# Optimization experiments

Measured on AMD Instinct MI355X. Metric: run time of the kernel, lower is better.

The kernel has to match this reference:

```python
import jax, jax.numpy as jnp
import numpy as np

N = 100000
IN_C = 128
OUT_C = 32
HEADS = 4
E = 1600000
NEG_SLOPE = 0.2


def setup_inputs() -> dict:
    key = jax.random.key(0)
    ks = jax.random.split(key, 8)
    x = jax.random.normal(ks[0], (N, IN_C), dtype=jnp.float32)
    edge_index = jax.random.randint(ks[1], (2, E), 0, N, dtype=jnp.int64)
    # GATConv params (PyG conventions): lin weight [H*C, in], att vectors [H, C], bias [H*C]
    sc = 1.0 / np.sqrt(IN_C)
    W = jax.random.uniform(ks[2], (HEADS * OUT_C, IN_C), dtype=jnp.float32, minval=-sc, maxval=sc)
    att_src = jax.random.normal(ks[3], (HEADS, OUT_C), dtype=jnp.float32) * 0.1
    att_dst = jax.random.normal(ks[4], (HEADS, OUT_C), dtype=jnp.float32) * 0.1
    bias_conv = jnp.zeros((HEADS * OUT_C,), dtype=jnp.float32)
    # final nn.Linear(H*C, C)
    sl = 1.0 / np.sqrt(HEADS * OUT_C)
    W_lin = jax.random.uniform(ks[5], (OUT_C, HEADS * OUT_C), dtype=jnp.float32, minval=-sl, maxval=sl)
    b_lin = jax.random.uniform(ks[6], (OUT_C,), dtype=jnp.float32, minval=-sl, maxval=sl)
    return {"x": x, "edge_index": edge_index, "W": W, "att_src": att_src,
            "att_dst": att_dst, "bias_conv": bias_conv, "W_lin": W_lin, "b_lin": b_lin}


def reference(x, edge_index, W, att_src, att_dst, bias_conv, W_lin, b_lin):
    n = x.shape[0]
    # add self loops (PyG default)
    loops = jnp.arange(n, dtype=edge_index.dtype)
    src = jnp.concatenate([edge_index[0], loops])
    dst = jnp.concatenate([edge_index[1], loops])
    # linear projection, per-head split: [N, H, C]
    h = (x @ W.T).reshape(n, HEADS, OUT_C)
    # per-node attention logits
    a_src = jnp.einsum('nhc,hc->nh', h, att_src)  # [N, H]
    a_dst = jnp.einsum('nhc,hc->nh', h, att_dst)  # [N, H]
    e = a_src[src] + a_dst[dst]                   # [E', H]
    e = jax.nn.leaky_relu(e, NEG_SLOPE)
    # segment softmax over incoming edges per destination node
    m = jax.ops.segment_max(e, dst, num_segments=n)       # [N, H]
    e = jnp.exp(e - m[dst])
    s = jax.ops.segment_sum(e, dst, num_segments=n)       # [N, H]
    alpha = e / s[dst]                                    # [E', H]
    # scatter-aggregate alpha-weighted source features
    msg = alpha[:, :, None] * h[src]                      # [E', H, C]
    out = jax.ops.segment_sum(msg, dst, num_segments=n)   # [N, H, C]
    out = out.reshape(n, HEADS * OUT_C) + bias_conv
    # final linear + ELU
    return jax.nn.elu(out @ W_lin.T + b_lin)
```

## Files before the change

kernel.cpp:

```cpp
#include <hip/hip_runtime.h>
#include <hip/hip_fp16.h>
#include <cstdint>
#include <cstddef>

#define NHEADS 4
#define OUT_C 32
#define HC 128
#define IN_CH 128
#define NEG_SLOPE 0.2f
#define LDSPAD 136
#define KEDGE 4096

typedef _Float16 half8 __attribute__((ext_vector_type(8)));
typedef float floatx4 __attribute__((ext_vector_type(4)));

static inline size_t align256(size_t v) { return (v + 255) & ~(size_t)255; }

__device__ __forceinline__ float lrelu(float v) { return v > 0.f ? v : NEG_SLOPE * v; }

__device__ __forceinline__ float wred_sum(float v) {
    v += __shfl_xor(v, 1);
    v += __shfl_xor(v, 2);
    v += __shfl_xor(v, 4);
    v += __shfl_xor(v, 8);
    v += __shfl_xor(v, 16);
    v += __shfl_xor(v, 32);
    return v;
}

__device__ __forceinline__ unsigned int pack_h2(float a, float b) {
    __half2 h = __floats2half2_rn(a, b);
    return *reinterpret_cast<unsigned int*>(&h);
}
__device__ __forceinline__ float2 unpack_h2(unsigned int u) {
    __half2 h = *reinterpret_cast<__half2*>(&u);
    return __half22float2(h);
}

__device__ __forceinline__ int detect_f64(const int* __restrict__ ei, int E, int* sf) {
    int t = threadIdx.x;
    if (t == 0) *sf = 0;
    __syncthreads();
    int lim = E < 1024 ? E : 1024;
    int acc = 0;
    for (int i = t; i < lim; i += 256) acc |= ei[2 * i + 1];
    acc |= __shfl_xor(acc, 1);
    acc |= __shfl_xor(acc, 2);
    acc |= __shfl_xor(acc, 4);
    acc |= __shfl_xor(acc, 8);
    acc |= __shfl_xor(acc, 16);
    acc |= __shfl_xor(acc, 32);
    if ((t & 63) == 0 && acc) atomicOr(sf, 1);
    __syncthreads();
    return *sf == 0;
}

__global__ __launch_bounds__(256) void gemm_hist(const float* __restrict__ x,
                                                 const float* __restrict__ W,
                                                 const float* __restrict__ att_src,
                                                 const float* __restrict__ att_dst,
                                                 __half* __restrict__ h,
                                                 float* __restrict__ a_src,
                                                 float* __restrict__ a_dst, int n,
                                                 const int* __restrict__ ei,
                                                 int* __restrict__ bcount,
                                                 int E, int sh, int GB) {
    __shared__ __align__(16) _Float16 Ws[128 * LDSPAD];
    __shared__ __align__(16) _Float16 Xs[128 * LDSPAD];
    __shared__ int hc[256];
    __shared__ int sf;
    int tid = threadIdx.x;

    if (blockIdx.x >= GB) {
        hc[tid] = 0;
        int f64 = detect_f64(ei, E, &sf);
        int nbh = gridDim.x - GB;
        int stride = nbh * 256;
        for (int i = (blockIdx.x - GB) * 256 + tid; i < E; i += stride) {
            int d;
            if (f64) d = (int)((const long long*)ei)[(size_t)E + i];
            else     d = ei[(size_t)E + i];
            atomicAdd(&hc[d >> sh], 1);
        }
        __syncthreads();
        if (hc[tid]) atomicAdd(&bcount[tid], hc[tid]);
        return;
    }
    int rowbase = blockIdx.x << 7;

    const float4* wf = (const float4*)W;
#pragma unroll
    for (int i = 0; i < 16; ++i) {
        int u = (i << 8) + tid;
        int r = u >> 5, g = u & 31;
        float4 v = wf[u];
        uint2 uu;
        uu.x = pack_h2(v.x, v.y);
        uu.y = pack_h2(v.z, v.w);
        *(uint2*)&Ws[r * LDSPAD + (g << 2)] = uu;
    }
    const float4* x4 = (const float4*)x;
#pragma unroll
    for (int i = 0; i < 16; ++i) {
        int u = (i << 8) + tid;
        int r = u >> 5, c4 = u & 31;
        int row = rowbase + r;
        if (row >= n) row = n - 1;
        float4 v = x4[((size_t)row << 5) + c4];
        uint2 uu;
        uu.x = pack_h2(v.x, v.y);
        uu.y = pack_h2(v.z, v.w);
        *(uint2*)&Xs[r * LDSPAD + (c4 << 2)] = uu;
    }
    __syncthreads();

    int lane = tid & 63, w = tid >> 6;
    int quad = lane >> 4, Lm = lane & 15;
    floatx4 acc[2][8];
#pragma unroll
    for (int rt = 0; rt < 2; ++rt)
#pragma unroll
        for (int c = 0; c < 8; ++c) acc[rt][c] = (floatx4){0.f, 0.f, 0.f, 0.f};

#pragma unroll
    for (int kc = 0; kc < 128; kc += 32) {
        int ko = kc + (quad << 3);
        half8 a0 = *(const half8*)&Xs[((w << 5) + Lm) * LDSPAD + ko];
        half8 a1 = *(const half8*)&Xs[((w << 5) + 16 + Lm) * LDSPAD + ko];
#pragma unroll
        for (int c = 0; c < 8; ++c) {
            half8 b = *(const half8*)&Ws[((c << 4) + Lm) * LDSPAD + ko];
            acc[0][c] = __builtin_amdgcn_mfma_f32_16x16x32_f16(a0, b, acc[0][c], 0, 0, 0);
            acc[1][c] = __builtin_amdgcn_mfma_f32_16x16x32_f16(a1, b, acc[1][c], 0, 0, 0);
        }
    }
    __syncthreads();
#pragma unroll
    for (int rt = 0; rt < 2; ++rt)
#pragma unroll
        for (int c = 0; c < 8; ++c)
#pragma unroll
            for (int i = 0; i < 4; ++i) {
                int rl = (w << 5) + (rt << 4) + (quad << 2) + i;
                int cl = (c << 4) + Lm;
                Xs[rl * LDSPAD + cl] = (_Float16)acc[rt][c][i];
            }
    __syncthreads();
#pragma unroll
    for (int i = 0; i < 8; ++i) {
        int u = (i << 8) + tid;
        int r = u >> 4, g = u & 15;
        int row = rowbase + r;
        if (row < n) {
            uint4 v = *(uint4*)&Xs[r * LDSPAD + (g << 3)];
            *(uint4*)(h + ((size_t)row << 7) + (g << 3)) = v;
        }
    }
    int r = tid >> 1, seg = tid & 1;
    int row = rowbase + r;
    const _Float16* hp = &Xs[r * LDSPAD + (seg << 6)];
    float sa = 0.f, da = 0.f, sb = 0.f, db = 0.f;
#pragma unroll
    for (int g8 = 0; g8 < 8; ++g8) {
        half8 v = *(const half8*)&hp[g8 << 3];
        int co = (seg << 6) + (g8 << 3);
        float4 A1 = *(const float4*)&att_src[co];
        float4 A2 = *(const float4*)&att_src[co + 4];
        float4 D1 = *(const float4*)&att_dst[co];
        float4 D2 = *(const float4*)&att_dst[co + 4];
        float f0 = (float)v[0], f1 = (float)v[1], f2 = (float)v[2], f3 = (float)v[3];
        float f4 = (float)v[4], f5 = (float)v[5], f6 = (float)v[6], f7 = (float)v[7];
        float ts = f0 * A1.x + f1 * A1.y + f2 * A1.z + f3 * A1.w
                 + f4 * A2.x + f5 * A2.y + f6 * A2.z + f7 * A2.w;
        float td = f0 * D1.x + f1 * D1.y + f2 * D1.z + f3 * D1.w
                 + f4 * D2.x + f5 * D2.y + f6 * D2.z + f7 * D2.w;
        if (g8 < 4) { sa += ts; da += td; } else { sb += ts; db += td; }
    }
    if (row < n) {
        int base = (row << 2) + (seg << 1);
        a_src[base] = sa;
        a_src[base + 1] = sb;
        a_dst[base] = da;
        a_dst[base + 1] = db;
    }
}

__global__ __launch_bounds__(256) void bscatter(const int* __restrict__ ei,
                                                const int* __restrict__ bcount,
                                                int* __restrict__ gcursor,
                                                int2* __restrict__ bkt,
                                                int E, int n, int sh) {
    __shared__ int cnt[256], base[256], lcur[256], ts[256];
    __shared__ int sf;
    int t = threadIdx.x;
    cnt[t] = 0;
    lcur[t] = 0;
    int f64 = detect_f64(ei, E, &sf);
    int total = E + n;
    int i0 = blockIdx.x * KEDGE;
    int ed[16], es[16];
#pragma unroll
    for (int j = 0; j < 16; ++j) {
        int i = i0 + (j << 8) + t;
        int s = 0, d = -1;
        if (i < total) {
            if (i < E) {
                if (f64) {
                    s = (int)((const long long*)ei)[i];
                    d = (int)((const long long*)ei)[(size_t)E + i];
                } else {
                    s = ei[i];
                    d = ei[(size_t)E + i];
                }
            } else {
                s = d = i - E;
            }
            atomicAdd(&cnt[d >> sh], 1);
        }
        ed[j] = d;
        es[j] = s;
    }
    int lo = t << sh, hi = (t + 1) << sh;
    if (hi > n) hi = n;
    int nodes = hi > lo ? hi - lo : 0;
    int v = bcount[t] + nodes;
    ts[t] = v;
    __syncthreads();
    int run = v;
    for (int d = 1; d < 256; d <<= 1) {
        int o = (t >= d) ? ts[t - d] : 0;
        __syncthreads();
        run += o;
        ts[t] = run;
        __syncthreads();
    }
    int excl = run - v;
    base[t] = excl + (cnt[t] ? atomicAdd(&gcursor[t], cnt[t]) : 0);
    __syncthreads();
#pragma unroll
    for (int j = 0; j < 16; ++j) {
        int d = ed[j];
        if (d >= 0) {
            int b = d >> sh;
            int pos = base[b] + atomicAdd(&lcur[b], 1);
            bkt[pos] = make_int2(d, es[j]);
        }
    }
}

__global__ __launch_bounds__(256) void bsort(const int2* __restrict__ bkt,
                                             const int* __restrict__ bcount,
                                             int* __restrict__ off,
                                             int* __restrict__ sorted,
                                             int n, int E, int sh) {
    __shared__ int cnt[512], offl[512], ts[256];
    int t = threadIdx.x, bid = blockIdx.x;
    int lo = t << sh, hi = (t + 1) << sh;
    if (hi > n) hi = n;
    int nodes = hi > lo ? hi - lo : 0;
    int v = bcount[t] + nodes;
    ts[t] = v;
    __syncthreads();
    int run = v;
    for (int d = 1; d < 256; d <<= 1) {
        int o = (t >= d) ? ts[t - d] : 0;
        __syncthreads();
        run += o;
        ts[t] = run;
        __syncthreads();
    }
    int e0 = (bid > 0) ? ts[bid - 1] : 0;
    int e1 = ts[bid];
    if (bid == gridDim.x - 1 && t == 0) off[n] = E + n;
    int node0 = bid << sh;
    int node1 = (bid + 1) << sh;
    if (node1 > n) node1 = n;
    int nn = node1 - node0;
    __syncthreads();
    cnt[t] = 0;
    cnt[t + 256] = 0;
    __syncthreads();
    for (int i = e0 + t; i < e1; i += 256) {
        int2 e = bkt[i];
        atomicAdd(&cnt[e.x - node0], 1);
    }
    __syncthreads();
    int a = cnt[t << 1], b = cnt[(t << 1) + 1];
    int s = a + b;
    ts[t] = s;
    __syncthreads();
    run = s;
    for (int d = 1; d < 256; d <<= 1) {
        int o = (t >= d) ? ts[t - d] : 0;
        __syncthreads();
        run += o;
        ts[t] = run;
        __syncthreads();
    }
    int excl = run - s;
    offl[t << 1] = excl;
    offl[(t << 1) + 1] = excl + a;
    cnt[t << 1] = 0;
    cnt[(t << 1) + 1] = 0;
    __syncthreads();
    for (int i = t; i < nn; i += 256) off[node0 + i] = e0 + offl[i];
    for (int i = e0 + t; i < e1; i += 256) {
        int2 e = bkt[i];
        int li = e.x - node0;
        int pos = e0 + offl[li] + atomicAdd(&cnt[li], 1);
        sorted[pos] = e.y;
    }
}

__device__ __forceinline__ void accum_half(const int* ssrc, const float* sal,
                                           const __half* __restrict__ h,
                                           int deg, int half, int L, int head,
                                           float4& acc) {
    float4 a0 = {0, 0, 0, 0}, a1 = {0, 0, 0, 0}, a2 = {0, 0, 0, 0}, a3 = {0, 0, 0, 0};
    int j = half;
    for (; j + 14 < deg; j += 16) {
        int s0 = ssrc[j], s1 = ssrc[j + 2], s2 = ssrc[j + 4], s3 = ssrc[j + 6];
        int s4 = ssrc[j + 8], s5 = ssrc[j + 10], s6 = ssrc[j + 12], s7 = ssrc[j + 14];
        float w0 = sal[(j << 2) + head];
        float w1 = sal[((j + 2) << 2) + head];
        float w2 = sal[((j + 4) << 2) + head];
        float w3 = sal[((j + 6) << 2) + head];
        float w4 = sal[((j + 8) << 2) + head];
        float w5 = sal[((j + 10) << 2) + head];
        float w6 = sal[((j + 12) << 2) + head];
        float w7 = sal[((j + 14) << 2) + head];
        uint2 u0 = *(const uint2*)(h + ((size_t)s0 << 7) + (L << 2));
        uint2 u1 = *(const uint2*)(h + ((size_t)s1 << 7) + (L << 2));
        uint2 u2 = *(const uint2*)(h + ((size_t)s2 << 7) + (L << 2));
        uint2 u3 = *(const uint2*)(h + ((size_t)s3 << 7) + (L << 2));
        uint2 u4 = *(const uint2*)(h + ((size_t)s4 << 7) + (L << 2));
        uint2 u5 = *(const uint2*)(h + ((size_t)s5 << 7) + (L << 2));
        uint2 u6 = *(const uint2*)(h + ((size_t)s6 << 7) + (L << 2));
        uint2 u7 = *(const uint2*)(h + ((size_t)s7 << 7) + (L << 2));
        float2 fa, fb;
        fa = unpack_h2(u0.x); fb = unpack_h2(u0.y);
        a0.x = fmaf(w0, fa.x, a0.x); a0.y = fmaf(w0, fa.y, a0.y);
        a0.z = fmaf(w0, fb.x, a0.z); a0.w = fmaf(w0, fb.y, a0.w);
        fa = unpack_h2(u1.x); fb = unpack_h2(u1.y);
        a1.x = fmaf(w1, fa.x, a1.x); a1.y = fmaf(w1, fa.y, a1.y);
        a1.z = fmaf(w1, fb.x, a1.z); a1.w = fmaf(w1, fb.y, a1.w);
        fa = unpack_h2(u2.x); fb = unpack_h2(u2.y);
        a2.x = fmaf(w2, fa.x, a2.x); a2.y = fmaf(w2, fa.y, a2.y);
        a2.z = fmaf(w2, fb.x, a2.z); a2.w = fmaf(w2, fb.y, a2.w);
        fa = unpack_h2(u3.x); fb = unpack_h2(u3.y);
        a3.x = fmaf(w3, fa.x, a3.x); a3.y = fmaf(w3, fa.y, a3.y);
        a3.z = fmaf(w3, fb.x, a3.z); a3.w = fmaf(w3, fb.y, a3.w);
        fa = unpack_h2(u4.x); fb = unpack_h2(u4.y);
        a0.x = fmaf(w4, fa.x, a0.x); a0.y = fmaf(w4, fa.y, a0.y);
        a0.z = fmaf(w4, fb.x, a0.z); a0.w = fmaf(w4, fb.y, a0.w);
        fa = unpack_h2(u5.x); fb = unpack_h2(u5.y);
        a1.x = fmaf(w5, fa.x, a1.x); a1.y = fmaf(w5, fa.y, a1.y);
        a1.z = fmaf(w5, fb.x, a1.z); a1.w = fmaf(w5, fb.y, a1.w);
        fa = unpack_h2(u6.x); fb = unpack_h2(u6.y);
        a2.x = fmaf(w6, fa.x, a2.x); a2.y = fmaf(w6, fa.y, a2.y);
        a2.z = fmaf(w6, fb.x, a2.z); a2.w = fmaf(w6, fb.y, a2.w);
        fa = unpack_h2(u7.x); fb = unpack_h2(u7.y);
        a3.x = fmaf(w7, fa.x, a3.x); a3.y = fmaf(w7, fa.y, a3.y);
        a3.z = fmaf(w7, fb.x, a3.z); a3.w = fmaf(w7, fb.y, a3.w);
    }
    for (; j + 6 < deg; j += 8) {
        int s0 = ssrc[j], s1 = ssrc[j + 2], s2 = ssrc[j + 4], s3 = ssrc[j + 6];
        float w0 = sal[(j << 2) + head];
        float w1 = sal[((j + 2) << 2) + head];
        float w2 = sal[((j + 4) << 2) + head];
        float w3 = sal[((j + 6) << 2) + head];
        uint2 u0 = *(const uint2*)(h + ((size_t)s0 << 7) + (L << 2));
        uint2 u1 = *(const uint2*)(h + ((size_t)s1 << 7) + (L << 2));
        uint2 u2 = *(const uint2*)(h + ((size_t)s2 << 7) + (L << 2));
        uint2 u3 = *(const uint2*)(h + ((size_t)s3 << 7) + (L << 2));
        float2 fa, fb;
        fa = unpack_h2(u0.x); fb = unpack_h2(u0.y);
        a0.x = fmaf(w0, fa.x, a0.x); a0.y = fmaf(w0, fa.y, a0.y);
        a0.z = fmaf(w0, fb.x, a0.z); a0.w = fmaf(w0, fb.y, a0.w);
        fa = unpack_h2(u1.x); fb = unpack_h2(u1.y);
        a1.x = fmaf(w1, fa.x, a1.x); a1.y = fmaf(w1, fa.y, a1.y);
        a1.z = fmaf(w1, fb.x, a1.z); a1.w = fmaf(w1, fb.y, a1.w);
        fa = unpack_h2(u2.x); fb = unpack_h2(u2.y);
        a2.x = fmaf(w2, fa.x, a2.x); a2.y = fmaf(w2, fa.y, a2.y);
        a2.z = fmaf(w2, fb.x, a2.z); a2.w = fmaf(w2, fb.y, a2.w);
        fa = unpack_h2(u3.x); fb = unpack_h2(u3.y);
        a3.x = fmaf(w3, fa.x, a3.x); a3.y = fmaf(w3, fa.y, a3.y);
        a3.z = fmaf(w3, fb.x, a3.z); a3.w = fmaf(w3, fb.y, a3.w);
    }
    for (; j < deg; j += 2) {
        int s0 = ssrc[j];
        float w0 = sal[(j << 2) + head];
        uint2 u0 = *(const uint2*)(h + ((size_t)s0 << 7) + (L << 2));
        float2 fa = unpack_h2(u0.x), fb = unpack_h2(u0.y);
        a0.x = fmaf(w0, fa.x, a0.x); a0.y = fmaf(w0, fa.y, a0.y);
        a0.z = fmaf(w0, fb.x, a0.z); a0.w = fmaf(w0, fb.y, a0.w);
    }
    acc.x += (a0.x + a1.x) + (a2.x + a3.x);
    acc.y += (a0.y + a1.y) + (a2.y + a3.y);
    acc.z += (a0.z + a1.z) + (a2.z + a3.z);
    acc.w += (a0.w + a1.w) + (a2.w + a3.w);
}

__global__ __launch_bounds__(256) void aggregate(const __half* __restrict__ h,
                                                 const int* __restrict__ sorted,
                                                 const int* __restrict__ off,
                                                 const float* __restrict__ a_src,
                                                 const float* __restrict__ a_dst,
                                                 const float* __restrict__ bias,
                                                 __half* __restrict__ agg, int n) {
    __shared__ __align__(16) int sh_src[4][64];
    __shared__ __align__(16) float sh_al[4][256];
    int wslot = threadIdx.x >> 6;
    int lane = threadIdx.x & 63;
    int wid = blockIdx.x * 4 + wslot;
    int nw = gridDim.x * 4;
    int L = lane & 31, half = lane >> 5, head = L >> 3;
    float4 b4 = ((const float4*)bias)[L];
    const float4* as4 = (const float4*)a_src;
    const float4* ad4 = (const float4*)a_dst;
    int* ssrc = sh_src[wslot];
    float* sal = sh_al[wslot];

    for (int node = wid; node < n; node += nw) {
        int start = off[node], end = off[node + 1];
        int deg = end - start;
        float4 ad = ad4[node];
        float4 acc = {0.f, 0.f, 0.f, 0.f};
        float4 psum = {0.f, 0.f, 0.f, 0.f};

        if (deg <= 64) {
            bool v = lane < deg;
            int idx = start + (v ? lane : 0);
            int s = sorted[idx];
            float4 as = as4[s];
            float4 p;
            p.x = v ? __expf(lrelu(as.x + ad.x)) : 0.f;
            p.y = v ? __expf(lrelu(as.y + ad.y)) : 0.f;
            p.z = v ? __expf(lrelu(as.z + ad.z)) : 0.f;
            p.w = v ? __expf(lrelu(as.w + ad.w)) : 0.f;
            psum = p;
            ssrc[lane] = s;
            *(float4*)&sal[lane << 2] = p;
            asm volatile("s_waitcnt lgkmcnt(0)" ::: "memory");
            accum_half(ssrc, sal, h, deg, half, L, head, acc);
            asm volatile("" ::: "memory");
        } else {
            for (int bb = 0; bb < deg; bb += 64) {
                int i = bb + lane;
                bool v = i < deg;
                int idx = start + (v ? i : 0);
                int s = sorted[idx];
                float4 as = as4[s];
                float4 p;
                p.x = v ? __expf(lrelu(as.x + ad.x)) : 0.f;
                p.y = v ? __expf(lrelu(as.y + ad.y)) : 0.f;
                p.z = v ? __expf(lrelu(as.z + ad.z)) : 0.f;
                p.w = v ? __expf(lrelu(as.w + ad.w)) : 0.f;
                psum.x += p.x; psum.y += p.y; psum.z += p.z; psum.w += p.w;
                ssrc[lane] = s;
                *(float4*)&sal[lane << 2] = p;
                asm volatile("s_waitcnt lgkmcnt(0)" ::: "memory");
                int cl = deg - bb;
                if (cl > 64) cl = 64;
                accum_half(ssrc, sal, h, cl, half, L, head, acc);
                asm volatile("" ::: "memory");
            }
        }
        float s0 = wred_sum(psum.x), s1 = wred_sum(psum.y);
        float s2 = wred_sum(psum.z), s3 = wred_sum(psum.w);
        float sh = (head == 0) ? s0 : (head == 1) ? s1 : (head == 2) ? s2 : s3;
        float inv = 1.f / sh;
        acc.x += __shfl_xor(acc.x, 32);
        acc.y += __shfl_xor(acc.y, 32);
        acc.z += __shfl_xor(acc.z, 32);
        acc.w += __shfl_xor(acc.w, 32);
        if (lane < 32) {
            float4 res = {fmaf(acc.x, inv, b4.x), fmaf(acc.y, inv, b4.y),
                          fmaf(acc.z, inv, b4.z), fmaf(acc.w, inv, b4.w)};
            uint2 u;
            u.x = pack_h2(res.x, res.y);
            u.y = pack_h2(res.z, res.w);
            *(uint2*)(agg + ((size_t)node << 7) + (L << 2)) = u;
        }
    }
}

__global__ __launch_bounds__(256) void proj(const __half* __restrict__ agg,
                                            const float* __restrict__ W_lin,
                                            const float* __restrict__ b_lin,
                                            float* __restrict__ out, int n) {
    __shared__ float xs[64][132];
    __shared__ float wt[128][36];
    int tid = threadIdx.x;
    const float4* w4 = (const float4*)W_lin;
#pragma unroll
    for (int i = 0; i < 4; ++i) {
        int f4 = (i << 8) + tid;
        int o = f4 >> 5, kk = (f4 & 31) << 2;
        float4 w = w4[f4];
        wt[kk][o] = w.x;
        wt[kk + 1][o] = w.y;
        wt[kk + 2][o] = w.z;
        wt[kk + 3][o] = w.w;
    }
    int rowbase = blockIdx.x << 6;
    const uint4* a4 = (const uint4*)agg;
#pragma unroll
    for (int i = 0; i < 4; ++i) {
        int f8 = (i << 8) + tid;
        int r = f8 >> 4, cc = (f8 & 15) << 3;
        int row = rowbase + r;
        if (row >= n) row = n - 1;
        uint4 u = a4[((size_t)row << 4) + (cc >> 3)];
        float2 f0 = unpack_h2(u.x), f1 = unpack_h2(u.y);
        float2 f2 = unpack_h2(u.z), f3 = unpack_h2(u.w);
        float* xp = &xs[r][cc];
        xp[0] = f0.x; xp[1] = f0.y; xp[2] = f1.x; xp[3] = f1.y;
        xp[4] = f2.x; xp[5] = f2.y; xp[6] = f3.x; xp[7] = f3.y;
    }
    __syncthreads();
    int r = tid >> 2, cg = tid & 3, c0 = cg << 3;
    float acc[8];
#pragma unroll
    for (int j = 0; j < 8; ++j) acc[j] = 0.f;
    for (int k = 0; k < 128; k += 4) {
        float4 xv = *(const float4*)&xs[r][k];
        float xk[4] = {xv.x, xv.y, xv.z, xv.w};
#pragma unroll
        for (int kk = 0; kk < 4; ++kk) {
            float4 wa = *(const float4*)&wt[k + kk][c0];
            float4 wb = *(const float4*)&wt[k + kk][c0 + 4];
            acc[0] = fmaf(xk[kk], wa.x, acc[0]);
            acc[1] = fmaf(xk[kk], wa.y, acc[1]);
            acc[2] = fmaf(xk[kk], wa.z, acc[2]);
            acc[3] = fmaf(xk[kk], wa.w, acc[3]);
            acc[4] = fmaf(xk[kk], wb.x, acc[4]);
            acc[5] = fmaf(xk[kk], wb.y, acc[5]);
            acc[6] = fmaf(xk[kk], wb.z, acc[6]);
            acc[7] = fmaf(xk[kk], wb.w, acc[7]);
        }
    }
    int row = rowbase + r;
    if (row < n) {
        float res[8];
#pragma unroll
        for (int j = 0; j < 8; ++j) {
            float v = acc[j] + b_lin[c0 + j];
            res[j] = v > 0.f ? v : (__expf(v) - 1.f);
        }
        float4* op = (float4*)(out + (size_t)row * 32 + c0);
        op[0] = make_float4(res[0], res[1], res[2], res[3]);
        op[1] = make_float4(res[4], res[5], res[6], res[7]);
    }
}

extern "C" void kernel_launch(void* const* d_in, const int* in_sizes, int n_in,
                              void* d_out, int out_size, void* d_ws, size_t ws_size,
                              hipStream_t stream) {
    const float* x = (const float*)d_in[0];
    const int* ei = (const int*)d_in[1];
    const float* W = (const float*)d_in[2];
    const float* att_src = (const float*)d_in[3];
    const float* att_dst = (const float*)d_in[4];
    const float* bias_conv = (const float*)d_in[5];
    const float* W_lin = (const float*)d_in[6];
    const float* b_lin = (const float*)d_in[7];
    int n = in_sizes[0] / IN_CH;
    int E = in_sizes[1] / 2;

    int sh = 0;
    while (((n + (1 << sh) - 1) >> sh) > 256) sh++;
    int NB = (n + (1 << sh) - 1) >> sh;

    char* ws = (char*)d_ws;
    size_t o = 0;
    auto alloc = [&](size_t bytes) { char* p = ws + o; o = align256(o + bytes); return p; };
    __half* h      = (__half*)alloc((size_t)n * HC * 2);
    __half* agg    = (__half*)alloc((size_t)n * HC * 2);
    float* a_src   = (float*)alloc((size_t)n * NHEADS * 4);
    float* a_dst   = (float*)alloc((size_t)n * NHEADS * 4);
    int* off       = (int*)alloc(((size_t)n + 1) * 4);
    int* bcount    = (int*)alloc(256 * 4);
    int* gcursor   = (int*)alloc(256 * 4);
    int* sorted    = (int*)alloc((size_t)(E + n + 64) * 4);
    int2* bkt      = (int2*)alloc((size_t)(E + n + 64) * 8);

    hipMemsetAsync(bcount, 0, 2048, stream);

    int GB = (n + 127) / 128;
    int NBH = 1024;
    gemm_hist<<<GB + NBH, 256, 0, stream>>>(x, W, att_src, att_dst, h, a_src, a_dst, n,
                                            ei, bcount, E, sh, GB);
    bscatter<<<(E + n + KEDGE - 1) / KEDGE, 256, 0, stream>>>(ei, bcount, gcursor, bkt, E, n, sh);
    bsort<<<NB, 256, 0, stream>>>(bkt, bcount, off, sorted, n, E, sh);
    aggregate<<<2048, 256, 0, stream>>>(h, sorted, off, a_src, a_dst, bias_conv, agg, n);
    proj<<<(n + 63) / 64, 256, 0, stream>>>(agg, W_lin, b_lin, (float*)d_out, n);
}
```

Baseline: 294.6 us.

## Precompute edge attention weights in bsort and store packed edge records

Moves the per-edge attention logit computation (a_src gather, leaky-relu, exp) from the aggregate kernel into the bucket sort kernel. The sort writes 16-byte records holding the source index and fp16-packed exp weights, with a_dst staged in shared memory. Aggregate then reads one contiguous record instead of a dependent random gather of a_src, which removes a latency chain from the hot loop. In exchange the sorted buffer grows from 4 to 16 bytes per edge, so more memory traffic, and the unnormalized weights are stored in fp16 without the max subtraction, so large logits could overflow.

Measured after the change: 307.0 us. +4.2%, slower.

```diff
diff --git a/kernel.cpp b/kernel.cpp
--- a/kernel.cpp
+++ b/kernel.cpp
@@ -250,10 +250,13 @@
 
 __global__ __launch_bounds__(256) void bsort(const int2* __restrict__ bkt,
                                              const int* __restrict__ bcount,
+                                             const float* __restrict__ a_src,
+                                             const float* __restrict__ a_dst,
                                              int* __restrict__ off,
-                                             int* __restrict__ sorted,
+                                             int4* __restrict__ recs,
                                              int n, int E, int sh) {
     __shared__ int cnt[512], offl[512], ts[256];
+    __shared__ __align__(16) float sad[512 * 4];
     int t = threadIdx.x, bid = blockIdx.x;
     int lo = t << sh, hi = (t + 1) << sh;
     if (hi > n) hi = n;
@@ -279,6 +282,9 @@
     __syncthreads();
     cnt[t] = 0;
     cnt[t + 256] = 0;
+    const float4* ad4 = (const float4*)a_dst;
+    for (int i = t; i < nn; i += 256)
+        *(float4*)&sad[i << 2] = ad4[node0 + i];
     __syncthreads();
     for (int i = e0 + t; i < e1; i += 256) {
         int2 e = bkt[i];
@@ -304,11 +310,19 @@
     cnt[(t << 1) + 1] = 0;
     __syncthreads();
     for (int i = t; i < nn; i += 256) off[node0 + i] = e0 + offl[i];
+    const float4* as4 = (const float4*)a_src;
     for (int i = e0 + t; i < e1; i += 256) {
         int2 e = bkt[i];
         int li = e.x - node0;
+        float4 as = as4[e.y];
+        float4 ad = *(const float4*)&sad[li << 2];
+        int4 rec;
+        rec.x = e.y;
+        rec.y = (int)pack_h2(__expf(lrelu(as.x + ad.x)), __expf(lrelu(as.y + ad.y)));
+        rec.z = (int)pack_h2(__expf(lrelu(as.z + ad.z)), __expf(lrelu(as.w + ad.w)));
+        rec.w = 0;
         int pos = e0 + offl[li] + atomicAdd(&cnt[li], 1);
-        sorted[pos] = e.y;
+        recs[pos] = rec;
     }
 }
 
@@ -402,10 +416,8 @@
 }
 
 __global__ __launch_bounds__(256) void aggregate(const __half* __restrict__ h,
-                                                 const int* __restrict__ sorted,
+                                                 const int4* __restrict__ recs,
                                                  const int* __restrict__ off,
-                                                 const float* __restrict__ a_src,
-                                                 const float* __restrict__ a_dst,
                                                  const float* __restrict__ bias,
                                                  __half* __restrict__ agg, int n) {
     __shared__ __align__(16) int sh_src[4][64];
@@ -416,30 +428,25 @@
     int nw = gridDim.x * 4;
     int L = lane & 31, half = lane >> 5, head = L >> 3;
     float4 b4 = ((const float4*)bias)[L];
-    const float4* as4 = (const float4*)a_src;
-    const float4* ad4 = (const float4*)a_dst;
     int* ssrc = sh_src[wslot];
     float* sal = sh_al[wslot];
 
     for (int node = wid; node < n; node += nw) {
         int start = off[node], end = off[node + 1];
         int deg = end - start;
-        float4 ad = ad4[node];
         float4 acc = {0.f, 0.f, 0.f, 0.f};
         float4 psum = {0.f, 0.f, 0.f, 0.f};
 
         if (deg <= 64) {
             bool v = lane < deg;
             int idx = start + (v ? lane : 0);
-            int s = sorted[idx];
-            float4 as = as4[s];
-            float4 p;
-            p.x = v ? __expf(lrelu(as.x + ad.x)) : 0.f;
-            p.y = v ? __expf(lrelu(as.y + ad.y)) : 0.f;
-            p.z = v ? __expf(lrelu(as.z + ad.z)) : 0.f;
-            p.w = v ? __expf(lrelu(as.w + ad.w)) : 0.f;
+            int4 rec = recs[idx];
+            float2 pa = unpack_h2((unsigned)rec.y);
+            float2 pb = unpack_h2((unsigned)rec.z);
+            float4 p = {pa.x, pa.y, pb.x, pb.y};
+            if (!v) p = make_float4(0.f, 0.f, 0.f, 0.f);
             psum = p;
-            ssrc[lane] = s;
+            ssrc[lane] = rec.x;
             *(float4*)&sal[lane << 2] = p;
             asm volatile("s_waitcnt lgkmcnt(0)" ::: "memory");
             accum_half(ssrc, sal, h, deg, half, L, head, acc);
@@ -449,15 +456,13 @@
                 int i = bb + lane;
                 bool v = i < deg;
                 int idx = start + (v ? i : 0);
-                int s = sorted[idx];
-                float4 as = as4[s];
-                float4 p;
-                p.x = v ? __expf(lrelu(as.x + ad.x)) : 0.f;
-                p.y = v ? __expf(lrelu(as.y + ad.y)) : 0.f;
-                p.z = v ? __expf(lrelu(as.z + ad.z)) : 0.f;
-                p.w = v ? __expf(lrelu(as.w + ad.w)) : 0.f;
+                int4 rec = recs[idx];
+                float2 pa = unpack_h2((unsigned)rec.y);
+                float2 pb = unpack_h2((unsigned)rec.z);
+                float4 p = {pa.x, pa.y, pb.x, pb.y};
+                if (!v) p = make_float4(0.f, 0.f, 0.f, 0.f);
                 psum.x += p.x; psum.y += p.y; psum.z += p.z; psum.w += p.w;
-                ssrc[lane] = s;
+                ssrc[lane] = rec.x;
                 *(float4*)&sal[lane << 2] = p;
                 asm volatile("s_waitcnt lgkmcnt(0)" ::: "memory");
                 int cl = deg - bb;
@@ -582,7 +587,7 @@
     int* off       = (int*)alloc(((size_t)n + 1) * 4);
     int* bcount    = (int*)alloc(256 * 4);
     int* gcursor   = (int*)alloc(256 * 4);
-    int* sorted    = (int*)alloc((size_t)(E + n + 64) * 4);
+    int4* recs     = (int4*)alloc((size_t)(E + n + 64) * 16);
     int2* bkt      = (int2*)alloc((size_t)(E + n + 64) * 8);
 
     hipMemsetAsync(bcount, 0, 2048, stream);
@@ -592,7 +597,7 @@
     gemm_hist<<<GB + NBH, 256, 0, stream>>>(x, W, att_src, att_dst, h, a_src, a_dst, n,
                                             ei, bcount, E, sh, GB);
     bscatter<<<(E + n + KEDGE - 1) / KEDGE, 256, 0, stream>>>(ei, bcount, gcursor, bkt, E, n, sh);
-    bsort<<<NB, 256, 0, stream>>>(bkt, bcount, off, sorted, n, E, sh);
-    aggregate<<<2048, 256, 0, stream>>>(h, sorted, off, a_src, a_dst, bias_conv, agg, n);
+    bsort<<<NB, 256, 0, stream>>>(bkt, bcount, a_src, a_dst, off, recs, n, E, sh);
+    aggregate<<<2048, 256, 0, stream>>>(h, recs, off, bias_conv, agg, n);
     proj<<<(n + 63) / 64, 256, 0, stream>>>(agg, W_lin, b_lin, (float*)d_out, n);
 }
```
